# Kernel optimization log

Hardware: AMD Instinct MI355X
Metric: run time of the kernel (lower is better)

The kernel has to match this reference:

```python
import jax, jax.numpy as jnp
import numpy as np

N = 50000      # num_nodes
E = 800000     # num_edges (avg degree 16)
D = 128        # input_dim = hidden_dim = output_dim
L = 3          # num_layers
EPS = 1e-5     # BatchNorm eps


def setup_inputs() -> dict:
    key = jax.random.key(0)
    k_x, k_e, k_w, k_b = jax.random.split(key, 4)
    x = jax.random.normal(k_x, (N, D), dtype=jnp.float32)
    edge_index = jax.random.randint(k_e, (2, E), 0, N, dtype=jnp.int32)
    # Stacked per-layer params: GCN weight/bias + BatchNorm gamma/beta
    Ws = jax.random.normal(k_w, (L, D, D), dtype=jnp.float32) * (1.0 / np.sqrt(D))
    bs = jax.random.normal(k_b, (L, D), dtype=jnp.float32) * 0.01
    gammas = jnp.ones((L, D), dtype=jnp.float32)
    betas = jnp.zeros((L, D), dtype=jnp.float32)
    return {"x": x, "edge_index": edge_index, "Ws": Ws, "bs": bs,
            "gammas": gammas, "betas": betas}


def reference(x, edge_index, Ws, bs, gammas, betas):
    """CausalGNN forward: L x (GCNConv -> BN(train stats) -> ReLU[not last]) with residuals.
    Dropout p=0 (deterministic). GCNConv is PyG-style: add self-loops, symmetric
    D^{-1/2} (A+I) D^{-1/2} normalization, linear transform + bias."""
    src, dst = edge_index[0], edge_index[1]
    # degree including self-loop (+1), computed at aggregation index
    deg = jax.ops.segment_sum(jnp.ones((E,), jnp.float32), dst, num_segments=N) + 1.0
    dis = jax.lax.rsqrt(deg)                       # deg >= 1, safe
    norm = dis[src] * dis[dst]                      # [E] edge norm
    self_norm = dis * dis                           # [N] self-loop norm = 1/deg

    for i in range(L):
        h = x @ Ws[i]                               # [N, D]
        # scatter-add aggregation of normalized neighbor messages
        agg = jax.ops.segment_sum(h[src] * norm[:, None], dst, num_segments=N)
        agg = agg + self_norm[:, None] * h + bs[i]
        # BatchNorm1d (training mode: biased batch statistics over nodes)
        mean = jnp.mean(agg, axis=0)
        var = jnp.mean(jnp.square(agg - mean), axis=0)
        y = gammas[i] * (agg - mean) * jax.lax.rsqrt(var + EPS) + betas[i]
        if i < L - 1:
            y = jax.nn.relu(y)
        x = x + y if i > 0 else y                   # residual (dims match)
    return x
```

## Files before the change

### kernel.cpp

```cpp
#include <hip/hip_runtime.h>
#include <hip/hip_bf16.h>
#include <hip/hip_fp16.h>

#define N_ 50000
#define E_ 800000
#define D_ 128
#define L_ 3

#define GG 782
#define NB 391
#define BCAP 3072
#define PB 200
#define PE 4000

typedef _Float16 half8 __attribute__((ext_vector_type(8)));
typedef float f32x4 __attribute__((ext_vector_type(4)));


__device__ inline float4 hcvt(uint2 u) {
    __half2 h0 = *(__half2*)&u.x;
    __half2 h1 = *(__half2*)&u.y;
    float2 f0 = __half22float2(h0);
    float2 f1 = __half22float2(h1);
    return make_float4(f0.x, f0.y, f1.x, f1.y);
}

__device__ inline unsigned pkh(float a, float b) {
    __half2 h = __floats2half2_rn(a, b);
    return *(unsigned*)&h;
}

__device__ inline unsigned short pkh1(float a) {
    _Float16 h = (_Float16)a;
    return *(unsigned short*)&h;
}


__global__ __launch_bounds__(256) void k_part(const int* __restrict__ src,
                                              const int* __restrict__ dst,
                                              const float* __restrict__ Ws,
                                              unsigned short* __restrict__ Wb,
                                              int* __restrict__ bucket_cnt,
                                              unsigned int* __restrict__ binned) {
    int b = blockIdx.x;
    if (b >= PB) {
        int l = b - PB;
        const float* Wl = Ws + l * 16384;
        unsigned short* Wo = Wb + l * 16384;
        for (int i = threadIdx.x; i < 16384; i += 256) {
            int n = i >> 7, k = i & 127;
            Wo[n * 128 + k] = pkh1(Wl[k * 128 + n]);
        }
        return;
    }
    __shared__ int hcnt[NB];
    __shared__ int hbase[NB];
    int t = threadIdx.x;
    for (int i = t; i < NB; i += 256) hcnt[i] = 0;
    __syncthreads();
    int e0 = b * PE;
    int dreg[16], sreg[16], oreg[16];
#pragma unroll
    for (int it = 0; it < 16; ++it) {
        int i = t + it * 256;
        if (i < PE) {
            int e = e0 + i;
            int d = dst[e];
            dreg[it] = d;
            sreg[it] = src[e];
            oreg[it] = atomicAdd(&hcnt[d >> 7], 1);
        }
    }
    __syncthreads();
    for (int i = t; i < NB; i += 256) {
        int c = hcnt[i];
        hbase[i] = c ? atomicAdd(&bucket_cnt[i], c) : 0;
    }
    __syncthreads();
#pragma unroll
    for (int it = 0; it < 16; ++it) {
        int i = t + it * 256;
        if (i < PE) {
            int d = dreg[it];
            int bk = d >> 7;
            binned[bk * BCAP + hbase[bk] + oreg[it]] =
                ((unsigned)(d & 127) << 16) | (unsigned)sreg[it];
        }
    }
}


__global__ __launch_bounds__(512) void k_bscan(const int* __restrict__ bucket_cnt,
                                               int* __restrict__ bucket_base,
                                               int* __restrict__ row_ptr) {
    __shared__ int wsum[8];
    int t = threadIdx.x;
    int lane = t & 63, wid = t >> 6;
    int v = (t < NB) ? bucket_cnt[t] : 0;
    int inc = v;
#pragma unroll
    for (int o = 1; o < 64; o <<= 1) {
        int u = __shfl_up(inc, o);
        if (lane >= o) inc += u;
    }
    if (lane == 63) wsum[wid] = inc;
    __syncthreads();
    if (wid == 0) {
        int w = (lane < 8) ? wsum[lane] : 0;
#pragma unroll
        for (int o = 1; o < 8; o <<= 1) {
            int u = __shfl_up(w, o);
            if (lane >= o) w += u;
        }
        if (lane < 8) wsum[lane] = w;
    }
    __syncthreads();
    int woff = wid ? wsum[wid - 1] : 0;
    if (t < NB) bucket_base[t] = inc + woff - v;
    if (t == 0) row_ptr[N_] = E_;
}


__device__ __forceinline__ void bin_body(const unsigned int* __restrict__ binned,
                                         const int* __restrict__ bucket_cnt,
                                         const int* __restrict__ bucket_base,
                                         int* __restrict__ row_ptr,
                                         float* __restrict__ dis,
                                         int* __restrict__ csr_src, int b) {
    __shared__ int h[128];
    __shared__ int hs[128];
    __shared__ int wtot[2];
    int t = threadIdx.x;
    if (t < 128) h[t] = 0;
    __syncthreads();
    int cnt  = bucket_cnt[b];
    int base = bucket_base[b];
    const unsigned int* bp = binned + b * BCAP;
    unsigned int pk[12];
    int off[12];
#pragma unroll
    for (int it = 0; it < 12; ++it) {
        int i = t + it * 256;
        if (i < cnt) {
            unsigned int p = bp[i];
            pk[it] = p;
            off[it] = atomicAdd(&h[p >> 16], 1);
        }
    }
    __syncthreads();
    int v = (t < 128) ? h[t] : 0;
    int lane = t & 63, wid = t >> 6;
    int inc = v;
#pragma unroll
    for (int o = 1; o < 64; o <<= 1) {
        int u = __shfl_up(inc, o);
        if (lane >= o) inc += u;
    }
    if (lane == 63 && wid < 2) wtot[wid] = inc;
    __syncthreads();
    if (wid == 1) inc += wtot[0];
    if (t < 128) {
        hs[t] = inc - v;
        int node = b * 128 + t;
        if (node < N_) {
            dis[node] = rsqrtf((float)v + 1.0f);
            row_ptr[node] = base + (inc - v);
        }
    }
    __syncthreads();
#pragma unroll
    for (int it = 0; it < 12; ++it) {
        int i = t + it * 256;
        if (i < cnt) {
            unsigned int p = pk[it];
            csr_src[base + hs[p >> 16] + off[it]] = (int)(p & 0xFFFFu);
        }
    }
}


template <bool IN16>
__device__ __forceinline__ void gemm_body(const void* __restrict__ Xin,
                                          const unsigned short* __restrict__ Wb,
                                          const float* __restrict__ disp,
                                          uint4* __restrict__ Hb,
                                          const float* __restrict__ st,
                                          const float* __restrict__ gamma,
                                          const float* __restrict__ beta,
                                          const unsigned short* __restrict__ resH,
                                          unsigned short* __restrict__ xoutH,
                                          int blk) {
    __shared__ unsigned short wt[128 * 136];
    __shared__ unsigned short xb[64 * 136];
    __shared__ float sab[256];
    int t  = threadIdx.x;
    int r0 = blk * 64;

    if (st) {
        if (t < 128) {
            float s = 0.f, s2 = 0.f;
#pragma unroll
            for (int k = 0; k < 8; ++k) {
                s  += st[k * 256 + t];
                s2 += st[k * 256 + 128 + t];
            }
            float mean = s * (1.0f / N_);
            float var  = s2 * (1.0f / N_) - mean * mean;
            float a = gamma[t] * rsqrtf(var + 1e-5f);
            sab[t]       = a;
            sab[128 + t] = beta[t] - mean * a;
        }
        __syncthreads();
    }

#pragma unroll
    for (int j = 0; j < 8; ++j) {
        int i = t + 256 * j;
        int row = i >> 4, c16 = i & 15;
        *(uint4*)&wt[row * 136 + c16 * 8] = ((const uint4*)Wb)[i];
    }
#pragma unroll
    for (int j = 0; j < 8; ++j) {
        int g   = t + 256 * j;
        int row = g >> 5;
        int c4  = (g & 31) * 4;
        int gr  = r0 + row;
        float4 v = make_float4(0.f, 0.f, 0.f, 0.f);
        if (gr < N_) {
            if constexpr (IN16) {
                v = hcvt(*(const uint2*)((const unsigned short*)Xin + gr * 128 + c4));
            } else {
                v = *(const float4*)((const float*)Xin + gr * 128 + c4);
            }
            if (st) {
                v.x = fmaxf(sab[c4] * v.x + sab[128 + c4], 0.f);
                v.y = fmaxf(sab[c4 + 1] * v.y + sab[128 + c4 + 1], 0.f);
                v.z = fmaxf(sab[c4 + 2] * v.z + sab[128 + c4 + 2], 0.f);
                v.w = fmaxf(sab[c4 + 3] * v.w + sab[128 + c4 + 3], 0.f);
                if (resH) {
                    float4 rr = hcvt(*(const uint2*)(resH + gr * 128 + c4));
                    v.x += rr.x; v.y += rr.y; v.z += rr.z; v.w += rr.w;
                }
            }
        }
        uint2 p;
        p.x = pkh(v.x, v.y);
        p.y = pkh(v.z, v.w);
        if (st && gr < N_) *(uint2*)(xoutH + gr * 128 + c4) = p;
        *(uint2*)&xb[row * 136 + c4] = p;
    }
    __syncthreads();

    int wv   = t >> 6;
    int lane = t & 63;
    int ln   = lane & 15;
    int quad = lane >> 4;

    const unsigned short* arow = &xb[(wv * 16 + ln) * 136 + quad * 8];
    half8 af[4];
#pragma unroll
    for (int ks = 0; ks < 4; ++ks) af[ks] = *(const half8*)(arow + ks * 32);

    f32x4 acc[8];
#pragma unroll
    for (int ct = 0; ct < 8; ++ct) acc[ct] = (f32x4){0.f, 0.f, 0.f, 0.f};

#pragma unroll
    for (int ct = 0; ct < 8; ++ct) {
        const unsigned short* wp = &wt[(ct * 16 + ln) * 136 + quad * 8];
#pragma unroll
        for (int ks = 0; ks < 4; ++ks) {
            half8 bf = *(const half8*)(wp + ks * 32);
            acc[ct] = __builtin_amdgcn_mfma_f32_16x16x32_f16(af[ks], bf, acc[ct], 0, 0, 0);
        }
    }

    float dr[4] = {1.f, 1.f, 1.f, 1.f};
    if (disp) {
#pragma unroll
        for (int reg = 0; reg < 4; ++reg) {
            int r = r0 + wv * 16 + quad * 4 + reg;
            dr[reg] = disp[r < N_ ? r : (N_ - 1)];
        }
    }
    __syncthreads();
#pragma unroll
    for (int ct = 0; ct < 8; ++ct) {
#pragma unroll
        for (int reg = 0; reg < 4; ++reg) {
            int lrow = wv * 16 + quad * 4 + reg;
            xb[lrow * 136 + ct * 16 + ln] = pkh1(acc[ct][reg] * dr[reg]);
        }
    }
    __syncthreads();
#pragma unroll
    for (int j = 0; j < 4; ++j) {
        int i = t + 256 * j;
        int row = i >> 4, c16 = i & 15;
        int gr = r0 + row;
        if (gr < N_) Hb[gr * 16 + c16] = *(uint4*)&xb[row * 136 + c16 * 8];
    }
}


__global__ __launch_bounds__(256) void k_fillg(const unsigned int* __restrict__ binned,
                                               const int* __restrict__ bucket_cnt,
                                               const int* __restrict__ bucket_base,
                                               int* __restrict__ row_ptr,
                                               float* __restrict__ dis,
                                               int* __restrict__ csr_src,
                                               const float* __restrict__ x,
                                               const unsigned short* __restrict__ Wb,
                                               uint4* __restrict__ Hb) {
    int b = blockIdx.x;
    if (b < NB) {
        bin_body(binned, bucket_cnt, bucket_base, row_ptr, dis, csr_src, b);
    } else {
        gemm_body<false>(x, Wb, nullptr, Hb, nullptr, nullptr, nullptr, nullptr,
                         nullptr, b - NB);
    }
}


__global__ __launch_bounds__(256) void k_gemm(const unsigned short* __restrict__ Xin,
                                              const unsigned short* __restrict__ Wb,
                                              const float* __restrict__ disp,
                                              uint4* __restrict__ Hb,
                                              const float* __restrict__ st,
                                              const float* __restrict__ gamma,
                                              const float* __restrict__ beta,
                                              const unsigned short* __restrict__ resH,
                                              unsigned short* __restrict__ xoutH) {
    gemm_body<true>(Xin, Wb, disp, Hb, st, gamma, beta, resH, xoutH, blockIdx.x);
}


template <bool SCALED, bool OUT16>
__global__ __launch_bounds__(256) void k_agg(const uint4* __restrict__ Hb,
                                             const int* __restrict__ row_ptr,
                                             const int* __restrict__ csr_src,
                                             const float* __restrict__ dis,
                                             const float* __restrict__ bias,
                                             void* __restrict__ AGGout,
                                             float* __restrict__ stats2) {
    int tid  = threadIdx.x;
    int sub  = tid >> 4;
    int lane = tid & 15;
    int node = blockIdx.x * 16 + sub;

    int beg = row_ptr[node], end = row_ptr[node + 1];
    float dn = dis[node];
    uint4 su = Hb[node * 16 + lane];
    float4 f0s = hcvt(make_uint2(su.x, su.y));
    float4 f1s = hcvt(make_uint2(su.z, su.w));
    float4 acc0, acc1;
    if constexpr (SCALED) {
        acc0 = f0s; acc1 = f1s;
    } else {
        acc0.x = dn * f0s.x; acc0.y = dn * f0s.y; acc0.z = dn * f0s.z; acc0.w = dn * f0s.w;
        acc1.x = dn * f1s.x; acc1.y = dn * f1s.y; acc1.z = dn * f1s.z; acc1.w = dn * f1s.w;
    }

    for (int c = beg; c < end; c += 16) {
        int m = end - c; if (m > 16) m = 16;
        int idx = 0; float dsv = 0.f;
        if (lane < m) {
            idx = csr_src[c + lane];
            if constexpr (!SCALED) dsv = dis[idx];
        }
        int j = 0;
        for (; j + 8 <= m; j += 8) {
            int s[8]; float d[8]; uint4 a[8];
#pragma unroll
            for (int k = 0; k < 8; ++k) {
                s[k] = __shfl(idx, j + k, 16);
                if constexpr (!SCALED) d[k] = __shfl(dsv, j + k, 16);
            }
#pragma unroll
            for (int k = 0; k < 8; ++k) a[k] = Hb[s[k] * 16 + lane];
#pragma unroll
            for (int k = 0; k < 8; ++k) {
                float4 f0 = hcvt(make_uint2(a[k].x, a[k].y));
                float4 f1 = hcvt(make_uint2(a[k].z, a[k].w));
                if constexpr (SCALED) {
                    acc0.x += f0.x; acc0.y += f0.y; acc0.z += f0.z; acc0.w += f0.w;
                    acc1.x += f1.x; acc1.y += f1.y; acc1.z += f1.z; acc1.w += f1.w;
                } else {
                    acc0.x += d[k] * f0.x; acc0.y += d[k] * f0.y;
                    acc0.z += d[k] * f0.z; acc0.w += d[k] * f0.w;
                    acc1.x += d[k] * f1.x; acc1.y += d[k] * f1.y;
                    acc1.z += d[k] * f1.z; acc1.w += d[k] * f1.w;
                }
            }
        }
        for (; j + 4 <= m; j += 4) {
            int s[4]; float d[4]; uint4 a[4];
#pragma unroll
            for (int k = 0; k < 4; ++k) {
                s[k] = __shfl(idx, j + k, 16);
                if constexpr (!SCALED) d[k] = __shfl(dsv, j + k, 16);
            }
#pragma unroll
            for (int k = 0; k < 4; ++k) a[k] = Hb[s[k] * 16 + lane];
#pragma unroll
            for (int k = 0; k < 4; ++k) {
                float4 f0 = hcvt(make_uint2(a[k].x, a[k].y));
                float4 f1 = hcvt(make_uint2(a[k].z, a[k].w));
                if constexpr (SCALED) {
                    acc0.x += f0.x; acc0.y += f0.y; acc0.z += f0.z; acc0.w += f0.w;
                    acc1.x += f1.x; acc1.y += f1.y; acc1.z += f1.z; acc1.w += f1.w;
                } else {
                    acc0.x += d[k] * f0.x; acc0.y += d[k] * f0.y;
                    acc0.z += d[k] * f0.z; acc0.w += d[k] * f0.w;
                    acc1.x += d[k] * f1.x; acc1.y += d[k] * f1.y;
                    acc1.z += d[k] * f1.z; acc1.w += d[k] * f1.w;
                }
            }
        }
        for (; j < m; ++j) {
            int s0 = __shfl(idx, j, 16);
            float d0 = 0.f;
            if constexpr (!SCALED) d0 = __shfl(dsv, j, 16);
            uint4 a0 = Hb[s0 * 16 + lane];
            float4 f0 = hcvt(make_uint2(a0.x, a0.y));
            float4 f1 = hcvt(make_uint2(a0.z, a0.w));
            if constexpr (SCALED) {
                acc0.x += f0.x; acc0.y += f0.y; acc0.z += f0.z; acc0.w += f0.w;
                acc1.x += f1.x; acc1.y += f1.y; acc1.z += f1.z; acc1.w += f1.w;
            } else {
                acc0.x += d0 * f0.x; acc0.y += d0 * f0.y;
                acc0.z += d0 * f0.z; acc0.w += d0 * f0.w;
                acc1.x += d0 * f1.x; acc1.y += d0 * f1.y;
                acc1.z += d0 * f1.z; acc1.w += d0 * f1.w;
            }
        }
    }

    float4 b0 = *(const float4*)(bias + lane * 8);
    float4 b1 = *(const float4*)(bias + lane * 8 + 4);
    float4 r0, r1;
    r0.x = dn * acc0.x + b0.x; r0.y = dn * acc0.y + b0.y;
    r0.z = dn * acc0.z + b0.z; r0.w = dn * acc0.w + b0.w;
    r1.x = dn * acc1.x + b1.x; r1.y = dn * acc1.y + b1.y;
    r1.z = dn * acc1.z + b1.z; r1.w = dn * acc1.w + b1.w;

    if constexpr (OUT16) {
        uint4 p;
        p.x = pkh(r0.x, r0.y); p.y = pkh(r0.z, r0.w);
        p.z = pkh(r1.x, r1.y); p.w = pkh(r1.z, r1.w);
        ((uint4*)AGGout)[node * 16 + lane] = p;
    } else {
        ((float4*)AGGout)[node * 32 + lane * 2]     = r0;
        ((float4*)AGGout)[node * 32 + lane * 2 + 1] = r1;
    }

    __shared__ float sbuf[16][128];
    float4* sp = (float4*)&sbuf[sub][lane * 8];
    sp[0] = r0; sp[1] = r1;
    __syncthreads();
    if (tid < 128) {
        float s = 0.f, s2 = 0.f;
#pragma unroll
        for (int k = 0; k < 16; ++k) {
            float v = sbuf[k][tid];
            s += v; s2 += v * v;
        }
        float* stp = stats2 + (blockIdx.x & 7) * 256;
        atomicAdd(&stp[tid], s);
        atomicAdd(&stp[128 + tid], s2);
    }
}


__global__ __launch_bounds__(256) void k_normF(const float4* __restrict__ AGG,
                                               const unsigned short* __restrict__ resH,
                                               const float* __restrict__ st,
                                               const float* __restrict__ gamma,
                                               const float* __restrict__ beta,
                                               float4* __restrict__ OUT) {
    __shared__ float sab[256];
    int t = threadIdx.x;
    if (t < 128) {
        float s = 0.f, s2 = 0.f;
#pragma unroll
        for (int k = 0; k < 8; ++k) {
            s  += st[k * 256 + t];
            s2 += st[k * 256 + 128 + t];
        }
        float mean = s * (1.0f / N_);
        float var  = s2 * (1.0f / N_) - mean * mean;
        float a = gamma[t] * rsqrtf(var + 1e-5f);
        sab[t]       = a;
        sab[128 + t] = beta[t] - mean * a;
    }
    __syncthreads();
    for (int i = blockIdx.x * 256 + t; i < N_ * 32; i += gridDim.x * 256) {
        int f4 = (i & 31) * 4;
        float4 v = AGG[i];
        float4 rr = hcvt(((const uint2*)resH)[i]);
        v.x = sab[f4] * v.x + sab[128 + f4] + rr.x;
        v.y = sab[f4 + 1] * v.y + sab[128 + f4 + 1] + rr.y;
        v.z = sab[f4 + 2] * v.z + sab[128 + f4 + 2] + rr.z;
        v.w = sab[f4 + 3] * v.w + sab[128 + f4 + 3] + rr.w;
        OUT[i] = v;
    }
}


extern "C" void kernel_launch(void* const* d_in, const int* in_sizes, int n_in,
                              void* d_out, int out_size, void* d_ws, size_t ws_size,
                              hipStream_t stream) {
    const float* x      = (const float*)d_in[0];
    const int*   ei     = (const int*)d_in[1];
    const float* Ws     = (const float*)d_in[2];
    const float* bs     = (const float*)d_in[3];
    const float* gammas = (const float*)d_in[4];
    const float* betas  = (const float*)d_in[5];
    float* out = (float*)d_out;

    const int* src = ei;
    const int* dst = ei + E_;

    char* w = (char*)d_ws;
    float* stats2      = (float*)(w + 0);
    int*   bucket_cnt  = (int*)(w + 24576);
    int*   bucket_base = (int*)(w + 26144);
    int*   row_ptr     = (int*)(w + 27712);
    float* dis         = (float*)(w + 227728);
    int*   csr_src     = (int*)(w + 427728);
    uint4* Hb          = (uint4*)(w + 3627776);
    unsigned short* XBh = (unsigned short*)(w + 16427776);
    unsigned short* Wb  = (unsigned short*)(w + 29227776);

    unsigned short* AGG16 = (unsigned short*)out;
    float* AGG = out;

    unsigned int* binned = (unsigned int*)XBh;

    hipMemsetAsync(d_ws, 0, 26144, stream);

    k_part<<<PB + 3, 256, 0, stream>>>(src, dst, Ws, Wb, bucket_cnt, binned);
    k_bscan<<<1, 512, 0, stream>>>(bucket_cnt, bucket_base, row_ptr);
    k_fillg<<<NB + GG, 256, 0, stream>>>(binned, bucket_cnt, bucket_base, row_ptr,
                                         dis, csr_src, x, Wb, Hb);

    k_agg<false, true><<<N_ / 16, 256, 0, stream>>>(Hb, row_ptr, csr_src, dis, bs,
                                                    AGG16, stats2);
    k_gemm<<<GG, 256, 0, stream>>>(AGG16, Wb + 16384, dis, Hb,
                                   stats2, gammas, betas, nullptr, XBh);
    k_agg<true, true><<<N_ / 16, 256, 0, stream>>>(Hb, row_ptr, csr_src, dis, bs + D_,
                                                   AGG16, stats2 + 2048);
    k_gemm<<<GG, 256, 0, stream>>>(AGG16, Wb + 32768, dis, Hb,
                                   stats2 + 2048, gammas + D_, betas + D_, XBh, XBh);
    k_agg<true, false><<<N_ / 16, 256, 0, stream>>>(Hb, row_ptr, csr_src, dis, bs + 2 * D_,
                                                    AGG, stats2 + 4096);
    k_normF<<<1024, 256, 0, stream>>>((const float4*)AGG, XBh,
                                      stats2 + 4096, gammas + 2 * D_, betas + 2 * D_,
                                      (float4*)out);
}
```

Baseline: 268.7 us.

## Split fp16 feature matrix into four column-quarter planes for cache-friendly gathers

The GEMM now writes H as four separate column planes of 32 fp16 values each. The aggregation kernel assigns 8 lanes per node, 32 nodes per block, and loops over the four planes in turn, so each gather pass touches a 3.2 MB slice of H that is more likely to stay in L2/LLC. The cost is re-reading the CSR indices four times, extra block-level syncs, and more stats atomics per block.

```diff
diff --git a/kernel.cpp b/kernel.cpp
--- a/kernel.cpp
+++ b/kernel.cpp
@@ -12,6 +12,7 @@
 #define BCAP 3072
 #define PB 200
 #define PE 4000
+#define AB 1563
 
 typedef _Float16 half8 __attribute__((ext_vector_type(8)));
 typedef float f32x4 __attribute__((ext_vector_type(4)));
@@ -183,7 +184,7 @@
 __device__ __forceinline__ void gemm_body(const void* __restrict__ Xin,
                                           const unsigned short* __restrict__ Wb,
                                           const float* __restrict__ disp,
-                                          uint4* __restrict__ Hb,
+                                          uint4* __restrict__ Hq4,
                                           const float* __restrict__ st,
                                           const float* __restrict__ gamma,
                                           const float* __restrict__ beta,
@@ -298,7 +299,10 @@
         int i = t + 256 * j;
         int row = i >> 4, c16 = i & 15;
         int gr = r0 + row;
-        if (gr < N_) Hb[gr * 16 + c16] = *(uint4*)&xb[row * 136 + c16 * 8];
+        if (gr < N_) {
+            int q = c16 >> 2;
+            Hq4[(q * N_ + gr) * 4 + (c16 & 3)] = *(uint4*)&xb[row * 136 + c16 * 8];
+        }
     }
 }
 
@@ -311,12 +315,12 @@
                                                int* __restrict__ csr_src,
                                                const float* __restrict__ x,
                                                const unsigned short* __restrict__ Wb,
-                                               uint4* __restrict__ Hb) {
+                                               uint4* __restrict__ Hq4) {
     int b = blockIdx.x;
     if (b < NB) {
         bin_body(binned, bucket_cnt, bucket_base, row_ptr, dis, csr_src, b);
     } else {
-        gemm_body<false>(x, Wb, nullptr, Hb, nullptr, nullptr, nullptr, nullptr,
+        gemm_body<false>(x, Wb, nullptr, Hq4, nullptr, nullptr, nullptr, nullptr,
                          nullptr, b - NB);
     }
 }
@@ -325,149 +329,120 @@
 __global__ __launch_bounds__(256) void k_gemm(const unsigned short* __restrict__ Xin,
                                               const unsigned short* __restrict__ Wb,
                                               const float* __restrict__ disp,
-                                              uint4* __restrict__ Hb,
+                                              uint4* __restrict__ Hq4,
                                               const float* __restrict__ st,
                                               const float* __restrict__ gamma,
                                               const float* __restrict__ beta,
                                               const unsigned short* __restrict__ resH,
                                               unsigned short* __restrict__ xoutH) {
-    gemm_body<true>(Xin, Wb, disp, Hb, st, gamma, beta, resH, xoutH, blockIdx.x);
+    gemm_body<true>(Xin, Wb, disp, Hq4, st, gamma, beta, resH, xoutH, blockIdx.x);
 }
 
 
 template <bool SCALED, bool OUT16>
-__global__ __launch_bounds__(256) void k_agg(const uint4* __restrict__ Hb,
+__global__ __launch_bounds__(256) void k_agg(const uint2* __restrict__ Hq,
                                              const int* __restrict__ row_ptr,
                                              const int* __restrict__ csr_src,
                                              const float* __restrict__ dis,
                                              const float* __restrict__ bias,
                                              void* __restrict__ AGGout,
                                              float* __restrict__ stats2) {
+    __shared__ float sbuf[32][32];
     int tid  = threadIdx.x;
-    int sub  = tid >> 4;
-    int lane = tid & 15;
-    int node = blockIdx.x * 16 + sub;
-
-    int beg = row_ptr[node], end = row_ptr[node + 1];
-    float dn = dis[node];
-    uint4 su = Hb[node * 16 + lane];
-    float4 f0s = hcvt(make_uint2(su.x, su.y));
-    float4 f1s = hcvt(make_uint2(su.z, su.w));
-    float4 acc0, acc1;
-    if constexpr (SCALED) {
-        acc0 = f0s; acc1 = f1s;
-    } else {
-        acc0.x = dn * f0s.x; acc0.y = dn * f0s.y; acc0.z = dn * f0s.z; acc0.w = dn * f0s.w;
-        acc1.x = dn * f1s.x; acc1.y = dn * f1s.y; acc1.z = dn * f1s.z; acc1.w = dn * f1s.w;
-    }
-
-    for (int c = beg; c < end; c += 16) {
-        int m = end - c; if (m > 16) m = 16;
-        int idx = 0; float dsv = 0.f;
-        if (lane < m) {
-            idx = csr_src[c + lane];
-            if constexpr (!SCALED) dsv = dis[idx];
-        }
-        int j = 0;
-        for (; j + 8 <= m; j += 8) {
-            int s[8]; float d[8]; uint4 a[8];
-#pragma unroll
-            for (int k = 0; k < 8; ++k) {
-                s[k] = __shfl(idx, j + k, 16);
-                if constexpr (!SCALED) d[k] = __shfl(dsv, j + k, 16);
-            }
-#pragma unroll
-            for (int k = 0; k < 8; ++k) a[k] = Hb[s[k] * 16 + lane];
-#pragma unroll
-            for (int k = 0; k < 8; ++k) {
-                float4 f0 = hcvt(make_uint2(a[k].x, a[k].y));
-                float4 f1 = hcvt(make_uint2(a[k].z, a[k].w));
-                if constexpr (SCALED) {
-                    acc0.x += f0.x; acc0.y += f0.y; acc0.z += f0.z; acc0.w += f0.w;
-                    acc1.x += f1.x; acc1.y += f1.y; acc1.z += f1.z; acc1.w += f1.w;
-                } else {
-                    acc0.x += d[k] * f0.x; acc0.y += d[k] * f0.y;
-                    acc0.z += d[k] * f0.z; acc0.w += d[k] * f0.w;
-                    acc1.x += d[k] * f1.x; acc1.y += d[k] * f1.y;
-                    acc1.z += d[k] * f1.z; acc1.w += d[k] * f1.w;
+    int g    = tid >> 3;
+    int lane = tid & 7;
+    int node = blockIdx.x * 32 + g;
+    bool valid = node < N_;
+    int nd  = valid ? node : 0;
+    int beg = row_ptr[nd];
+    int end = valid ? row_ptr[nd + 1] : beg;
+    float dn = dis[nd];
+    float* stp = stats2 + (blockIdx.x & 7) * 256;
+
+    for (int q = 0; q < 4; ++q) {
+        const uint2* Hqq = Hq + (size_t)q * (N_ * 8);
+        float4 acc = make_float4(0.f, 0.f, 0.f, 0.f);
+        if (valid) {
+            float4 fs = hcvt(Hqq[node * 8 + lane]);
+            if constexpr (SCALED) {
+                acc = fs;
+            } else {
+                acc.x = dn * fs.x; acc.y = dn * fs.y;
+                acc.z = dn * fs.z; acc.w = dn * fs.w;
+            }
+        }
+        for (int c = beg; c < end; c += 8) {
+            int m = end - c; if (m > 8) m = 8;
+            int idx = 0; float dsv = 0.f;
+            if (lane < m) {
+                idx = csr_src[c + lane];
+                if constexpr (!SCALED) dsv = dis[idx];
+            }
+            if (m == 8) {
+                int s[8]; float d[8]; uint2 a[8];
+#pragma unroll
+                for (int k = 0; k < 8; ++k) {
+                    s[k] = __shfl(idx, k, 8);
+                    if constexpr (!SCALED) d[k] = __shfl(dsv, k, 8);
                 }
-            }
-        }
-        for (; j + 4 <= m; j += 4) {
-            int s[4]; float d[4]; uint4 a[4];
-#pragma unroll
-            for (int k = 0; k < 4; ++k) {
-                s[k] = __shfl(idx, j + k, 16);
-                if constexpr (!SCALED) d[k] = __shfl(dsv, j + k, 16);
-            }
-#pragma unroll
-            for (int k = 0; k < 4; ++k) a[k] = Hb[s[k] * 16 + lane];
-#pragma unroll
-            for (int k = 0; k < 4; ++k) {
-                float4 f0 = hcvt(make_uint2(a[k].x, a[k].y));
-                float4 f1 = hcvt(make_uint2(a[k].z, a[k].w));
-                if constexpr (SCALED) {
-                    acc0.x += f0.x; acc0.y += f0.y; acc0.z += f0.z; acc0.w += f0.w;
-                    acc1.x += f1.x; acc1.y += f1.y; acc1.z += f1.z; acc1.w += f1.w;
-                } else {
-                    acc0.x += d[k] * f0.x; acc0.y += d[k] * f0.y;
-                    acc0.z += d[k] * f0.z; acc0.w += d[k] * f0.w;
-                    acc1.x += d[k] * f1.x; acc1.y += d[k] * f1.y;
-                    acc1.z += d[k] * f1.z; acc1.w += d[k] * f1.w;
+#pragma unroll
+                for (int k = 0; k < 8; ++k) a[k] = Hqq[s[k] * 8 + lane];
+#pragma unroll
+                for (int k = 0; k < 8; ++k) {
+                    float4 f = hcvt(a[k]);
+                    if constexpr (SCALED) {
+                        acc.x += f.x; acc.y += f.y; acc.z += f.z; acc.w += f.w;
+                    } else {
+                        acc.x += d[k] * f.x; acc.y += d[k] * f.y;
+                        acc.z += d[k] * f.z; acc.w += d[k] * f.w;
+                    }
                 }
-            }
-        }
-        for (; j < m; ++j) {
-            int s0 = __shfl(idx, j, 16);
-            float d0 = 0.f;
-            if constexpr (!SCALED) d0 = __shfl(dsv, j, 16);
-            uint4 a0 = Hb[s0 * 16 + lane];
-            float4 f0 = hcvt(make_uint2(a0.x, a0.y));
-            float4 f1 = hcvt(make_uint2(a0.z, a0.w));
-            if constexpr (SCALED) {
-                acc0.x += f0.x; acc0.y += f0.y; acc0.z += f0.z; acc0.w += f0.w;
-                acc1.x += f1.x; acc1.y += f1.y; acc1.z += f1.z; acc1.w += f1.w;
             } else {
-                acc0.x += d0 * f0.x; acc0.y += d0 * f0.y;
-                acc0.z += d0 * f0.z; acc0.w += d0 * f0.w;
-                acc1.x += d0 * f1.x; acc1.y += d0 * f1.y;
-                acc1.z += d0 * f1.z; acc1.w += d0 * f1.w;
-            }
-        }
-    }
-
-    float4 b0 = *(const float4*)(bias + lane * 8);
-    float4 b1 = *(const float4*)(bias + lane * 8 + 4);
-    float4 r0, r1;
-    r0.x = dn * acc0.x + b0.x; r0.y = dn * acc0.y + b0.y;
-    r0.z = dn * acc0.z + b0.z; r0.w = dn * acc0.w + b0.w;
-    r1.x = dn * acc1.x + b1.x; r1.y = dn * acc1.y + b1.y;
-    r1.z = dn * acc1.z + b1.z; r1.w = dn * acc1.w + b1.w;
-
-    if constexpr (OUT16) {
-        uint4 p;
-        p.x = pkh(r0.x, r0.y); p.y = pkh(r0.z, r0.w);
-        p.z = pkh(r1.x, r1.y); p.w = pkh(r1.z, r1.w);
-        ((uint4*)AGGout)[node * 16 + lane] = p;
-    } else {
-        ((float4*)AGGout)[node * 32 + lane * 2]     = r0;
-        ((float4*)AGGout)[node * 32 + lane * 2 + 1] = r1;
-    }
-
-    __shared__ float sbuf[16][128];
-    float4* sp = (float4*)&sbuf[sub][lane * 8];
-    sp[0] = r0; sp[1] = r1;
-    __syncthreads();
-    if (tid < 128) {
-        float s = 0.f, s2 = 0.f;
-#pragma unroll
-        for (int k = 0; k < 16; ++k) {
-            float v = sbuf[k][tid];
-            s += v; s2 += v * v;
-        }
-        float* stp = stats2 + (blockIdx.x & 7) * 256;
-        atomicAdd(&stp[tid], s);
-        atomicAdd(&stp[128 + tid], s2);
+                for (int j = 0; j < m; ++j) {
+                    int s0 = __shfl(idx, j, 8);
+                    float d0 = 0.f;
+                    if constexpr (!SCALED) d0 = __shfl(dsv, j, 8);
+                    float4 f = hcvt(Hqq[s0 * 8 + lane]);
+                    if constexpr (SCALED) {
+                        acc.x += f.x; acc.y += f.y; acc.z += f.z; acc.w += f.w;
+                    } else {
+                        acc.x += d0 * f.x; acc.y += d0 * f.y;
+                        acc.z += d0 * f.z; acc.w += d0 * f.w;
+                    }
+                }
+            }
+        }
+
+        float4 r = make_float4(0.f, 0.f, 0.f, 0.f);
+        if (valid) {
+            const float* bq = bias + q * 32 + lane * 4;
+            r.x = dn * acc.x + bq[0];
+            r.y = dn * acc.y + bq[1];
+            r.z = dn * acc.z + bq[2];
+            r.w = dn * acc.w + bq[3];
+            if constexpr (OUT16) {
+                uint2 p;
+                p.x = pkh(r.x, r.y);
+                p.y = pkh(r.z, r.w);
+                ((uint2*)AGGout)[node * 32 + q * 8 + lane] = p;
+            } else {
+                ((float4*)AGGout)[node * 32 + q * 8 + lane] = r;
+            }
+        }
+
+        *(float4*)&sbuf[g][lane * 4] = r;
+        __syncthreads();
+        if (tid < 32) {
+            float s = 0.f, s2 = 0.f;
+#pragma unroll
+            for (int k = 0; k < 32; ++k) {
+                float v = sbuf[k][tid];
+                s += v; s2 += v * v;
+            }
+            atomicAdd(&stp[q * 32 + tid], s);
+            atomicAdd(&stp[128 + q * 32 + tid], s2);
+        }
+        __syncthreads();
     }
 }
 
@@ -528,7 +503,7 @@
     int*   row_ptr     = (int*)(w + 27712);
     float* dis         = (float*)(w + 227728);
     int*   csr_src     = (int*)(w + 427728);
-    uint4* Hb          = (uint4*)(w + 3627776);
+    uint4* Hq4         = (uint4*)(w + 3627776);
     unsigned short* XBh = (unsigned short*)(w + 16427776);
     unsigned short* Wb  = (unsigned short*)(w + 29227776);
 
@@ -542,18 +517,18 @@
     k_part<<<PB + 3, 256, 0, stream>>>(src, dst, Ws, Wb, bucket_cnt, binned);
     k_bscan<<<1, 512, 0, stream>>>(bucket_cnt, bucket_base, row_ptr);
     k_fillg<<<NB + GG, 256, 0, stream>>>(binned, bucket_cnt, bucket_base, row_ptr,
-                                         dis, csr_src, x, Wb, Hb);
-
-    k_agg<false, true><<<N_ / 16, 256, 0, stream>>>(Hb, row_ptr, csr_src, dis, bs,
-                                                    AGG16, stats2);
-    k_gemm<<<GG, 256, 0, stream>>>(AGG16, Wb + 16384, dis, Hb,
+                                         dis, csr_src, x, Wb, Hq4);
+
+    k_agg<false, true><<<AB, 256, 0, stream>>>((const uint2*)Hq4, row_ptr, csr_src,
+                                               dis, bs, AGG16, stats2);
+    k_gemm<<<GG, 256, 0, stream>>>(AGG16, Wb + 16384, dis, Hq4,
                                    stats2, gammas, betas, nullptr, XBh);
-    k_agg<true, true><<<N_ / 16, 256, 0, stream>>>(Hb, row_ptr, csr_src, dis, bs + D_,
-                                                   AGG16, stats2 + 2048);
-    k_gemm<<<GG, 256, 0, stream>>>(AGG16, Wb + 32768, dis, Hb,
+    k_agg<true, true><<<AB, 256, 0, stream>>>((const uint2*)Hq4, row_ptr, csr_src,
+                                              dis, bs + D_, AGG16, stats2 + 2048);
+    k_gemm<<<GG, 256, 0, stream>>>(AGG16, Wb + 32768, dis, Hq4,
                                    stats2 + 2048, gammas + D_, betas + D_, XBh, XBh);
-    k_agg<true, false><<<N_ / 16, 256, 0, stream>>>(Hb, row_ptr, csr_src, dis, bs + 2 * D_,
-                                                    AGG, stats2 + 4096);
+    k_agg<true, false><<<AB, 256, 0, stream>>>((const uint2*)Hq4, row_ptr, csr_src,
+                                               dis, bs + 2 * D_, AGG, stats2 + 4096);
     k_normF<<<1024, 256, 0, stream>>>((const float4*)AGG, XBh,
                                       stats2 + 4096, gammas + 2 * D_, betas + 2 * D_,
                                       (float4*)out);
```

Result: slower. 336.7 us (+25.3%).
